# Kernel tuning notes

Hardware: AMD Instinct MI355X
Metric: run time of the kernel (lower is better)

The kernel has to match this reference:

```python
import jax, jax.numpy as jnp
import numpy as np
from jax import lax

D_MODEL = 1024
D_IN = 1024        # expand=1 -> d_inner = d_model
N_STATE = 16       # d_state
DT_RANK = 64       # ceil(d_model/16)
D_FFN = 4096
BATCH, SEQ = 2, 2048


def setup_inputs() -> dict:
    key = jax.random.key(0)
    ks = jax.random.split(key, 12)
    r = lambda i, shape, s=0.02: jax.random.normal(ks[i], shape, jnp.float32) * s
    ones = lambda n: jnp.ones((n,), jnp.float32)
    zeros = lambda n: jnp.zeros((n,), jnp.float32)
    # S4D-real init for A
    A_log = jnp.log(jnp.tile(jnp.arange(1, N_STATE + 1, dtype=jnp.float32), (D_IN, 1)))
    return {
        "src": jax.random.normal(ks[0], (BATCH, SEQ, D_MODEL), jnp.float32),
        "in_proj_w": r(1, (2 * D_IN, D_MODEL)),
        "conv_w": r(2, (D_IN, 2), 0.5),
        "conv_b": zeros(D_IN),
        "x_proj_w": r(3, (DT_RANK + 2 * N_STATE, D_IN)),
        "dt_proj_w": r(4, (D_IN, DT_RANK), 0.1),
        "dt_proj_b": r(5, (D_IN,), 0.1),
        "A_log": A_log,
        "Dp": ones(D_IN),
        "out_proj_w": r(6, (D_MODEL, D_IN)),
        "mnorm_g": ones(D_MODEL), "mnorm_b": zeros(D_MODEL),
        "n1_g": ones(D_MODEL), "n1_b": zeros(D_MODEL),
        "n2_g": ones(D_MODEL), "n2_b": zeros(D_MODEL),
        "n3_g": ones(D_MODEL), "n3_b": zeros(D_MODEL),
        "ffn_w1": r(7, (D_FFN, D_MODEL)),
        "ffn_w2": r(8, (D_MODEL, D_FFN)),
        "fe_w": r(9, (D_MODEL, D_MODEL)),
        "fe_b": zeros(D_MODEL),
    }


def _ln(x, g, b, eps=1e-5):
    m = x.mean(-1, keepdims=True)
    v = ((x - m) ** 2).mean(-1, keepdims=True)
    return (x - m) / jnp.sqrt(v + eps) * g + b


def _mamba(x, in_proj_w, conv_w, conv_b, x_proj_w, dt_proj_w, dt_proj_b,
           A_log, Dp, out_proj_w):
    B, L, _ = x.shape
    xz = x @ in_proj_w.T                       # (B,L,2*D_IN)
    x_in, z = jnp.split(xz, 2, axis=-1)
    # depthwise causal conv1d, kernel size 2: y[l] = w0*x[l-1] + w1*x[l] + b
    x_prev = jnp.pad(x_in, ((0, 0), (1, 0), (0, 0)))[:, :L]
    x_c = jax.nn.silu(x_prev * conv_w[:, 0] + x_in * conv_w[:, 1] + conv_b)
    x_dbl = x_c @ x_proj_w.T                   # (B,L,DT_RANK+2N)
    dt, Bm, Cm = jnp.split(x_dbl, [DT_RANK, DT_RANK + N_STATE], axis=-1)
    delta = jax.nn.softplus(dt @ dt_proj_w.T + dt_proj_b)   # (B,L,D_IN)
    A = -jnp.exp(A_log)                        # (D_IN,N)
    deltaA = jnp.exp(delta[..., None] * A)                   # (B,L,D_IN,N)
    dBu = delta[..., None] * Bm[:, :, None, :] * x_c[..., None]

    def step(h, t):
        dA_t, dBu_t, C_t = t                   # (B,D_IN,N),(B,D_IN,N),(B,N)
        h = dA_t * h + dBu_t
        y = jnp.einsum('bdn,bn->bd', h, C_t)
        return h, y

    h0 = jnp.zeros((B, D_IN, N_STATE), x.dtype)
    _, ys = lax.scan(step, h0,
                     (deltaA.transpose(1, 0, 2, 3),
                      dBu.transpose(1, 0, 2, 3),
                      Cm.transpose(1, 0, 2)))
    y = ys.transpose(1, 0, 2)                  # (B,L,D_IN)
    y = (y + x_c * Dp) * jax.nn.silu(z)
    return y @ out_proj_w.T


def reference(src, in_proj_w, conv_w, conv_b, x_proj_w, dt_proj_w, dt_proj_b,
              A_log, Dp, out_proj_w, mnorm_g, mnorm_b, n1_g, n1_b, n2_g, n2_b,
              n3_g, n3_b, ffn_w1, ffn_w2, fe_w, fe_b):
    # src1 = MambaBlock(norm1(src)); dropout = identity (eval)
    h = _mamba(_ln(src, n1_g, n1_b), in_proj_w, conv_w, conv_b, x_proj_w,
               dt_proj_w, dt_proj_b, A_log, Dp, out_proj_w)
    src = src + _ln(h, mnorm_g, mnorm_b)
    # FFN: Linear -> LeakyReLU(0.01) -> Linear (no bias)
    f = _ln(src, n2_g, n2_b) @ ffn_w1.T
    f = jnp.where(f >= 0, f, 0.01 * f) @ ffn_w2.T
    src = src + f
    src = src + (_ln(src, n3_g, n3_b) @ fe_w.T + fe_b)
    return src
```

## Files before the change

kernel.cpp:

```cpp
#include <hip/hip_runtime.h>
#include <hip/hip_bf16.h>
#include <cstddef>

#define L_SEQ   2048
#define NBATCH  2
#define NROWS   (NBATCH * L_SEQ)
#define NSTATE  16
#define CH      64
#define NCHUNK  (L_SEQ / CH)

typedef __bf16 bf16x8 __attribute__((ext_vector_type(8)));
typedef float  f32x4  __attribute__((ext_vector_type(4)));
typedef unsigned short u16x4 __attribute__((ext_vector_type(4)));

static __device__ __forceinline__ unsigned short f2bf(float f) {
  unsigned int x = __builtin_bit_cast(unsigned int, f);
  x += 0x7fffu + ((x >> 16) & 1u);
  return (unsigned short)(x >> 16);
}
static __device__ __forceinline__ float bf2f(unsigned short u) {
  return __builtin_bit_cast(float, ((unsigned int)u) << 16);
}

#define GLDS(g, l) __builtin_amdgcn_global_load_lds( \
    (const __attribute__((address_space(1))) void*)(g), \
    (__attribute__((address_space(3))) void*)(l), 16, 0, 0)

#define DRAIN_VM() asm volatile("s_waitcnt vmcnt(0)" ::: "memory")

__global__ __launch_bounds__(256) void cvt_bf16_kernel(
    const float* __restrict__ in, unsigned short* __restrict__ out, int n4)
{
  const int i = blockIdx.x * 256 + threadIdx.x;
  if (i < n4) {
    const float4 v = reinterpret_cast<const float4*>(in)[i];
    u16x4 o;
    o[0] = f2bf(v.x); o[1] = f2bf(v.y); o[2] = f2bf(v.z); o[3] = f2bf(v.w);
    reinterpret_cast<u16x4*>(out)[i] = o;
  }
}

__global__ __launch_bounds__(256) void cvt_all_kernel(
    const float* __restrict__ ipw, const float* __restrict__ xpw,
    const float* __restrict__ dtw, const float* __restrict__ opw,
    const float* __restrict__ w1,  const float* __restrict__ w2,
    const float* __restrict__ few,
    unsigned short* __restrict__ o_ipw, unsigned short* __restrict__ o_xpw,
    unsigned short* __restrict__ o_dtw, unsigned short* __restrict__ o_opw,
    unsigned short* __restrict__ o_w1,  unsigned short* __restrict__ o_w2,
    unsigned short* __restrict__ o_few)
{
  int i = blockIdx.x * 256 + threadIdx.x;
  const float* src; unsigned short* dst;
  if (i < 524288)                 { src = ipw; dst = o_ipw; }
  else if ((i -= 524288) < 24576) { src = xpw; dst = o_xpw; }
  else if ((i -= 24576) < 16384)  { src = dtw; dst = o_dtw; }
  else if ((i -= 16384) < 262144) { src = opw; dst = o_opw; }
  else if ((i -= 262144) < 1048576){ src = w1; dst = o_w1; }
  else if ((i -= 1048576) < 1048576){ src = w2; dst = o_w2; }
  else if ((i -= 1048576) < 262144){ src = few; dst = o_few; }
  else return;
  const float4 v = reinterpret_cast<const float4*>(src)[i];
  u16x4 o;
  o[0] = f2bf(v.x); o[1] = f2bf(v.y); o[2] = f2bf(v.z); o[3] = f2bf(v.w);
  reinterpret_cast<u16x4*>(dst)[i] = o;
}

__global__ __launch_bounds__(256) void ln_kernel(
    const float* __restrict__ in, const float* __restrict__ g,
    const float* __restrict__ bta, const float* __restrict__ res,
    float* __restrict__ out, unsigned short* __restrict__ outb)
{
  const int row = blockIdx.x;
  const int tid = threadIdx.x;
  __shared__ float sm[8];
  const float4 v = reinterpret_cast<const float4*>(in + (size_t)row * 1024)[tid];
  float s = v.x + v.y + v.z + v.w;
#pragma unroll
  for (int o = 32; o > 0; o >>= 1) s += __shfl_down(s, o, 64);
  if ((tid & 63) == 0) sm[tid >> 6] = s;
  __syncthreads();
  const float mean = (sm[0] + sm[1] + sm[2] + sm[3]) * (1.f / 1024.f);
  const float dx = v.x - mean, dy = v.y - mean, dz = v.z - mean, dw = v.w - mean;
  float q = dx * dx + dy * dy + dz * dz + dw * dw;
#pragma unroll
  for (int o = 32; o > 0; o >>= 1) q += __shfl_down(q, o, 64);
  __syncthreads();
  if ((tid & 63) == 0) sm[tid >> 6] = q;
  __syncthreads();
  const float var = (sm[0] + sm[1] + sm[2] + sm[3]) * (1.f / 1024.f);
  const float rstd = rsqrtf(var + 1e-5f);
  const float4 gv = reinterpret_cast<const float4*>(g)[tid];
  const float4 bv = reinterpret_cast<const float4*>(bta)[tid];
  float4 o4;
  o4.x = dx * rstd * gv.x + bv.x;
  o4.y = dy * rstd * gv.y + bv.y;
  o4.z = dz * rstd * gv.z + bv.z;
  o4.w = dw * rstd * gv.w + bv.w;
  if (outb) {
    u16x4 ob;
    ob[0] = f2bf(o4.x); ob[1] = f2bf(o4.y); ob[2] = f2bf(o4.z); ob[3] = f2bf(o4.w);
    reinterpret_cast<u16x4*>(outb + (size_t)row * 1024)[tid] = ob;
  } else {
    if (res) {
      const float4 rv = reinterpret_cast<const float4*>(res + (size_t)row * 1024)[tid];
      o4.x += rv.x; o4.y += rv.y; o4.z += rv.z; o4.w += rv.w;
    }
    reinterpret_cast<float4*>(out + (size_t)row * 1024)[tid] = o4;
  }
}

__global__ __launch_bounds__(256) void gemm_bf16_kernel(
    const unsigned short* __restrict__ A, int lda,
    const unsigned short* __restrict__ B, int ldb,
    void* __restrict__ Cv, int ldc,
    const float* __restrict__ bias, const float* __restrict__ res,
    int K, int act, int outbf, int gy)
{
  __shared__ unsigned short As[2][128 * 32];
  __shared__ unsigned short Bs[2][128 * 32];
  const int t = threadIdx.x;
  const int w = t >> 6, l = t & 63;

  const int q = gridDim.x >> 3;
  const int nid = (blockIdx.x & 7) * q + (blockIdx.x >> 3);
  const int bm = (nid / gy) * 128;
  const int bn = (nid % gy) * 128;

  const int wr = (w >> 1) * 64, wc = (w & 1) * 64;
  f32x4 acc[4][4] = {};

  const int srow = t >> 2;
  const int sk = (t & 3) * 8;
  const unsigned short* gA0 = A + (size_t)(bm + srow) * lda + sk;
  const unsigned short* gA1 = gA0 + (size_t)64 * lda;
  const unsigned short* gB0 = B + (size_t)(bn + srow) * ldb + sk;
  const unsigned short* gB1 = gB0 + (size_t)64 * ldb;

  const int fr = l & 15;
  const int kb = (l >> 4) * 8;

#define STAGE(buf, k0) do { \
    GLDS(gA0 + (k0), &As[buf][w * 512]); \
    GLDS(gA1 + (k0), &As[buf][2048 + w * 512]); \
    GLDS(gB0 + (k0), &Bs[buf][w * 512]); \
    GLDS(gB1 + (k0), &Bs[buf][2048 + w * 512]); \
  } while (0)

#define COMPUTE(buf) do { \
    bf16x8 af[4], bfr[4]; \
    _Pragma("unroll") \
    for (int i = 0; i < 4; ++i) \
      af[i] = *reinterpret_cast<const bf16x8*>(&As[buf][(wr + i * 16 + fr) * 32 + kb]); \
    _Pragma("unroll") \
    for (int j = 0; j < 4; ++j) \
      bfr[j] = *reinterpret_cast<const bf16x8*>(&Bs[buf][(wc + j * 16 + fr) * 32 + kb]); \
    _Pragma("unroll") \
    for (int i = 0; i < 4; ++i) \
      _Pragma("unroll") \
      for (int j = 0; j < 4; ++j) \
        acc[i][j] = __builtin_amdgcn_mfma_f32_16x16x32_bf16(af[i], bfr[j], acc[i][j], 0, 0, 0); \
  } while (0)

  STAGE(0, 0);
  DRAIN_VM();
  __syncthreads();
  int cur = 0;
  for (int k0 = 32; k0 < K; k0 += 32) {
    __builtin_amdgcn_sched_barrier(0);
    STAGE(cur ^ 1, k0);
    __builtin_amdgcn_sched_barrier(0);
    COMPUTE(cur);
    DRAIN_VM();
    __syncthreads();
    cur ^= 1;
  }
  COMPUTE(cur);
#undef STAGE
#undef COMPUTE

  const int crow = (l >> 4) * 4;
  const int ccol = l & 15;
  float* Cf = (float*)Cv;
  unsigned short* Cb = (unsigned short*)Cv;
#pragma unroll
  for (int i = 0; i < 4; ++i) {
#pragma unroll
    for (int j = 0; j < 4; ++j) {
      const int n = bn + wc + j * 16 + ccol;
      const float bv = bias ? bias[n] : 0.f;
#pragma unroll
      for (int r = 0; r < 4; ++r) {
        const int m = bm + wr + i * 16 + crow + r;
        float v = acc[i][j][r] + bv;
        if (act == 1) v = (v > 20.f) ? v : __logf(1.f + __expf(v));
        else if (act == 2) v = (v >= 0.f) ? v : 0.01f * v;
        if (res) v += res[(size_t)m * ldc + n];
        if (outbf) Cb[(size_t)m * ldc + n] = f2bf(v);
        else       Cf[(size_t)m * ldc + n] = v;
      }
    }
  }
}

template<int BK>
__global__ __launch_bounds__(512) void gemm_ksplit_kernel(
    const unsigned short* __restrict__ A, int lda,
    const unsigned short* __restrict__ B, int ldb,
    void* __restrict__ Cv, int ldc,
    const float* __restrict__ bias, const float* __restrict__ res,
    int K, int act, int outbf, int gy)
{
  constexpr int ABYTES = 128 * BK * 2;
  constexpr int NISS = (BK == 32) ? 2 : 4;
  constexpr int RPI  = (BK == 32) ? 64 : 32;
  constexpr int NS   = BK / 32;
  __shared__ __align__(16) unsigned char smem[8 * ABYTES];
  const int tid = threadIdx.x;
  const int grp = tid >> 8;
  const int t = tid & 255;
  const int w = t >> 6, l = t & 63;

  const int q = gridDim.x >> 3;
  const int nid = (blockIdx.x & 7) * q + (blockIdx.x >> 3);
  const int bm = (nid / gy) * 128;
  const int bn = (nid % gy) * 128;

  const int K2 = K >> 1;
  const int koff = grp * K2;
  const int wr = (w >> 1) * 64, wc = (w & 1) * 64;
  f32x4 acc[4][4] = {};

  const int srow = (BK == 32) ? (t >> 2) : (t >> 3);
  const int sk   = (BK == 32) ? ((t & 3) * 8) : ((t & 7) * 8);
  const unsigned short* gA = A + (size_t)(bm + srow) * lda + koff + sk;
  const unsigned short* gB = B + (size_t)(bn + srow) * ldb + koff + sk;

  const int gbase = grp * 2 * ABYTES;
  const int fr = l & 15;
  const int kb = (l >> 4) * 8;

#define SAb(buf) (smem + gbase + (buf) * ABYTES)
#define SBb(buf) (smem + 4 * ABYTES + gbase + (buf) * ABYTES)

#define STAGEK(buf, k0) do { \
    _Pragma("unroll") \
    for (int ii = 0; ii < NISS; ++ii) { \
      GLDS(gA + (k0) + (size_t)ii * RPI * lda, SAb(buf) + ii * 4096 + w * 1024); \
      GLDS(gB + (k0) + (size_t)ii * RPI * ldb, SBb(buf) + ii * 4096 + w * 1024); \
    } \
  } while (0)

#define COMPUTEK(buf) do { \
    _Pragma("unroll") \
    for (int s = 0; s < NS; ++s) { \
      bf16x8 af[4], bfr[4]; \
      _Pragma("unroll") \
      for (int i = 0; i < 4; ++i) \
        af[i] = *reinterpret_cast<const bf16x8*>((const unsigned short*)SAb(buf) + (wr + i * 16 + fr) * BK + s * 32 + kb); \
      _Pragma("unroll") \
      for (int j = 0; j < 4; ++j) \
        bfr[j] = *reinterpret_cast<const bf16x8*>((const unsigned short*)SBb(buf) + (wc + j * 16 + fr) * BK + s * 32 + kb); \
      _Pragma("unroll") \
      for (int i = 0; i < 4; ++i) \
        _Pragma("unroll") \
        for (int j = 0; j < 4; ++j) \
          acc[i][j] = __builtin_amdgcn_mfma_f32_16x16x32_bf16(af[i], bfr[j], acc[i][j], 0, 0, 0); \
    } \
  } while (0)

  STAGEK(0, 0);
  DRAIN_VM();
  __syncthreads();
  int cur = 0;
  for (int k0 = BK; k0 < K2; k0 += BK) {
    __builtin_amdgcn_sched_barrier(0);
    STAGEK(cur ^ 1, k0);
    __builtin_amdgcn_sched_barrier(0);
    COMPUTEK(cur);
    DRAIN_VM();
    __syncthreads();
    cur ^= 1;
  }
  COMPUTEK(cur);
#undef STAGEK
#undef COMPUTEK
#undef SAb
#undef SBb

  __syncthreads();
  float* red = (float*)smem;
  if (grp) {
#pragma unroll
    for (int i = 0; i < 4; ++i)
#pragma unroll
      for (int j = 0; j < 4; ++j)
        *reinterpret_cast<f32x4*>(&red[(t << 6) + (i * 4 + j) * 4]) = acc[i][j];
  }
  __syncthreads();
  if (!grp) {
    const int crow = (l >> 4) * 4;
    const int ccol = l & 15;
    float* Cf = (float*)Cv;
    unsigned short* Cb = (unsigned short*)Cv;
#pragma unroll
    for (int i = 0; i < 4; ++i) {
#pragma unroll
      for (int j = 0; j < 4; ++j) {
        const f32x4 o = *reinterpret_cast<const f32x4*>(&red[(t << 6) + (i * 4 + j) * 4]);
        const int n = bn + wc + j * 16 + ccol;
        const float bv = bias ? bias[n] : 0.f;
#pragma unroll
        for (int r = 0; r < 4; ++r) {
          const int m = bm + wr + i * 16 + crow + r;
          float v = acc[i][j][r] + o[r] + bv;
          if (act == 1) v = (v > 20.f) ? v : __logf(1.f + __expf(v));
          else if (act == 2) v = (v >= 0.f) ? v : 0.01f * v;
          if (res) v += res[(size_t)m * ldc + n];
          if (outbf) Cb[(size_t)m * ldc + n] = f2bf(v);
          else       Cf[(size_t)m * ldc + n] = v;
        }
      }
    }
  }
}

__global__ __launch_bounds__(256) void xproj_kernel(
    const unsigned short* __restrict__ A, int lda,
    const unsigned short* __restrict__ B, int ldb,
    float* __restrict__ C)
{
  __shared__ unsigned short As[2][128 * 32];
  __shared__ unsigned short Bs[2][96 * 32];
  const int t = threadIdx.x;
  const int w = t >> 6, l = t & 63;
  const int bm = blockIdx.x * 128;
  const int kbase = blockIdx.y * 128;

  f32x4 acc[2][6] = {};

  const int srow = t >> 2;
  const int sk = (t & 3) * 8;
  const unsigned short* gA0 = A + (size_t)(bm + srow) * lda + kbase + sk;
  const unsigned short* gA1 = gA0 + (size_t)64 * lda;
  const unsigned short* gB0 = B + (size_t)srow * ldb + kbase + sk;
  const unsigned short* gB1 = gB0 + (size_t)64 * ldb;

  const int fr = l & 15;
  const int kb = (l >> 4) * 8;

#define STAGEX(buf, k0) do { \
    GLDS(gA0 + (k0), &As[buf][w * 512]); \
    GLDS(gA1 + (k0), &As[buf][2048 + w * 512]); \
    GLDS(gB0 + (k0), &Bs[buf][w * 512]); \
    if (w < 2) GLDS(gB1 + (k0), &Bs[buf][2048 + w * 512]); \
  } while (0)

#define COMPUTEX(buf) do { \
    bf16x8 af[2], bfr[6]; \
    _Pragma("unroll") \
    for (int i = 0; i < 2; ++i) \
      af[i] = *reinterpret_cast<const bf16x8*>(&As[buf][(w * 32 + i * 16 + fr) * 32 + kb]); \
    _Pragma("unroll") \
    for (int j = 0; j < 6; ++j) \
      bfr[j] = *reinterpret_cast<const bf16x8*>(&Bs[buf][(j * 16 + fr) * 32 + kb]); \
    _Pragma("unroll") \
    for (int i = 0; i < 2; ++i) \
      _Pragma("unroll") \
      for (int j = 0; j < 6; ++j) \
        acc[i][j] = __builtin_amdgcn_mfma_f32_16x16x32_bf16(af[i], bfr[j], acc[i][j], 0, 0, 0); \
  } while (0)

  STAGEX(0, 0);
  DRAIN_VM();
  __syncthreads();
  int cur = 0;
  for (int s = 1; s < 4; ++s) {
    __builtin_amdgcn_sched_barrier(0);
    STAGEX(cur ^ 1, s * 32);
    __builtin_amdgcn_sched_barrier(0);
    COMPUTEX(cur);
    DRAIN_VM();
    __syncthreads();
    cur ^= 1;
  }
  COMPUTEX(cur);
#undef STAGEX
#undef COMPUTEX

  const int crow = (l >> 4) * 4;
  const int ccol = l & 15;
#pragma unroll
  for (int i = 0; i < 2; ++i)
#pragma unroll
    for (int j = 0; j < 6; ++j)
#pragma unroll
      for (int r = 0; r < 4; ++r) {
        const int m = bm + w * 32 + i * 16 + crow + r;
        const int n = j * 16 + ccol;
        atomicAdd(&C[(size_t)m * 96 + n], acc[i][j][r]);
      }
}

__global__ __launch_bounds__(256) void conv_silu_kernel(
    const unsigned short* __restrict__ xz, const float* __restrict__ cw,
    const float* __restrict__ cb, float* __restrict__ xc,
    unsigned short* __restrict__ xcb)
{
  const int idx = blockIdx.x * 256 + threadIdx.x;
  const int row = idx >> 10;
  const int d = idx & 1023;
  const int l = row & (L_SEQ - 1);
  const float cur = bf2f(xz[(size_t)row * 2048 + d]);
  const float prev = (l == 0) ? 0.f : bf2f(xz[(size_t)(row - 1) * 2048 + d]);
  const float v = prev * cw[d * 2 + 0] + cur * cw[d * 2 + 1] + cb[d];
  const float sv = v / (1.f + __expf(-v));
  xc[idx] = sv;
  xcb[idx] = f2bf(sv);
}

__global__ __launch_bounds__(256) void scan_pass1(
    const float* __restrict__ delta, const float* __restrict__ xc,
    const float* __restrict__ xdbl, const float* __restrict__ A_log,
    float* __restrict__ hfin, float* __restrict__ pcum)
{
  const int tid = threadIdx.x;
  const int db = blockIdx.x & 3;
  const int c = (blockIdx.x >> 2) & (NCHUNK - 1);
  const int b = blockIdx.x >> 7;
  const int d = db * 256 + tid;
  __shared__ float Bsh[CH][16];
  {
    const int lr = tid >> 2, q = tid & 3;
    const float* p = xdbl + ((size_t)(b * L_SEQ + c * CH + lr) * 96) + 64 + q * 4;
    *reinterpret_cast<float4*>(&Bsh[lr][q * 4]) = *reinterpret_cast<const float4*>(p);
  }
  float a[NSTATE];
#pragma unroll
  for (int n = 0; n < NSTATE; ++n) a[n] = -__expf(A_log[d * 16 + n]);
  __syncthreads();
  float h[NSTATE], P[NSTATE];
#pragma unroll
  for (int n = 0; n < NSTATE; ++n) { h[n] = 0.f; P[n] = 1.f; }
  const size_t rowbase = (size_t)(b * L_SEQ + c * CH);
  for (int s = 0; s < CH; ++s) {
    const size_t row = rowbase + s;
    const float dl = delta[row * 1024 + d];
    const float xcv = xc[row * 1024 + d];
#pragma unroll
    for (int n = 0; n < NSTATE; ++n) {
      const float dA = __expf(dl * a[n]);
      h[n] = h[n] * dA + (dl * Bsh[s][n]) * xcv;
      P[n] *= dA;
    }
  }
  const size_t base = ((size_t)((b * NCHUNK + c) * 1024 + d)) * 16;
  float4* hp = reinterpret_cast<float4*>(hfin + base);
  float4* pp = reinterpret_cast<float4*>(pcum + base);
#pragma unroll
  for (int qq = 0; qq < 4; ++qq) {
    hp[qq] = make_float4(h[qq * 4], h[qq * 4 + 1], h[qq * 4 + 2], h[qq * 4 + 3]);
    pp[qq] = make_float4(P[qq * 4], P[qq * 4 + 1], P[qq * 4 + 2], P[qq * 4 + 3]);
  }
}

__global__ __launch_bounds__(256) void scan_pass2(
    const float* __restrict__ hfin, const float* __restrict__ pcum,
    float* __restrict__ hstart)
{
  const int t = blockIdx.x * 256 + threadIdx.x;
  const int b = t >> 14;
  const int dn = t & 16383;
  const size_t base = (size_t)b * NCHUNK * 16384 + dn;
  float h = 0.f;
  for (int c = 0; c < NCHUNK; ++c) {
    const size_t idx = base + (size_t)c * 16384;
    hstart[idx] = h;
    h = pcum[idx] * h + hfin[idx];
  }
}

__global__ __launch_bounds__(256) void scan_pass3(
    const float* __restrict__ delta, const float* __restrict__ xc,
    const float* __restrict__ xdbl, const float* __restrict__ A_log,
    const float* __restrict__ hstart, const float* __restrict__ Dp,
    const unsigned short* __restrict__ xz, unsigned short* __restrict__ yout)
{
  const int tid = threadIdx.x;
  const int db = blockIdx.x & 3;
  const int c = (blockIdx.x >> 2) & (NCHUNK - 1);
  const int b = blockIdx.x >> 7;
  const int d = db * 256 + tid;
  __shared__ float Bsh[CH][16];
  __shared__ float Csh[CH][16];
  {
    const int lr = tid >> 2, q = tid & 3;
    const float* p = xdbl + ((size_t)(b * L_SEQ + c * CH + lr) * 96);
    *reinterpret_cast<float4*>(&Bsh[lr][q * 4]) = *reinterpret_cast<const float4*>(p + 64 + q * 4);
    *reinterpret_cast<float4*>(&Csh[lr][q * 4]) = *reinterpret_cast<const float4*>(p + 80 + q * 4);
  }
  float a[NSTATE];
#pragma unroll
  for (int n = 0; n < NSTATE; ++n) a[n] = -__expf(A_log[d * 16 + n]);
  float h[NSTATE];
  {
    const size_t base = ((size_t)((b * NCHUNK + c) * 1024 + d)) * 16;
    const float4* hp = reinterpret_cast<const float4*>(hstart + base);
#pragma unroll
    for (int qq = 0; qq < 4; ++qq) {
      const float4 v = hp[qq];
      h[qq * 4] = v.x; h[qq * 4 + 1] = v.y; h[qq * 4 + 2] = v.z; h[qq * 4 + 3] = v.w;
    }
  }
  const float dpv = Dp[d];
  __syncthreads();
  const size_t rowbase = (size_t)(b * L_SEQ + c * CH);
  for (int s = 0; s < CH; ++s) {
    const size_t row = rowbase + s;
    const float dl = delta[row * 1024 + d];
    const float xcv = xc[row * 1024 + d];
    float y = 0.f;
#pragma unroll
    for (int n = 0; n < NSTATE; ++n) {
      const float dA = __expf(dl * a[n]);
      h[n] = h[n] * dA + (dl * Bsh[s][n]) * xcv;
      y += h[n] * Csh[s][n];
    }
    const float z = bf2f(xz[row * 2048 + 1024 + d]);
    const float sil = z / (1.f + __expf(-z));
    yout[row * 1024 + d] = f2bf((y + xcv * dpv) * sil);
  }
}

extern "C" void kernel_launch(void* const* d_in, const int* in_sizes, int n_in,
                              void* d_out, int out_size, void* d_ws, size_t ws_size,
                              hipStream_t stream)
{
  (void)in_sizes; (void)n_in; (void)out_size; (void)ws_size;
  const float* src        = (const float*)d_in[0];
  const float* in_proj_w  = (const float*)d_in[1];
  const float* conv_w     = (const float*)d_in[2];
  const float* conv_b     = (const float*)d_in[3];
  const float* x_proj_w   = (const float*)d_in[4];
  const float* dt_proj_w  = (const float*)d_in[5];
  const float* dt_proj_b  = (const float*)d_in[6];
  const float* A_log      = (const float*)d_in[7];
  const float* Dp         = (const float*)d_in[8];
  const float* out_proj_w = (const float*)d_in[9];
  const float* mnorm_g    = (const float*)d_in[10];
  const float* mnorm_b    = (const float*)d_in[11];
  const float* n1_g       = (const float*)d_in[12];
  const float* n1_b       = (const float*)d_in[13];
  const float* n2_g       = (const float*)d_in[14];
  const float* n2_b       = (const float*)d_in[15];
  const float* n3_g       = (const float*)d_in[16];
  const float* n3_b       = (const float*)d_in[17];
  const float* ffn_w1     = (const float*)d_in[18];
  const float* ffn_w2     = (const float*)d_in[19];
  const float* fe_w       = (const float*)d_in[20];
  const float* fe_b       = (const float*)d_in[21];
  float* out = (float*)d_out;
  float* ws  = (float*)d_ws;

  unsigned short* xzb  = (unsigned short*)ws;
  unsigned short* xdblb= (unsigned short*)(ws + 4194304);
  unsigned short* dtwb = (unsigned short*)(ws + 4390912);
  float* xc    = ws + 8388608;
  float* xdbl  = ws + 12582912;
  float* delta = ws + 13107200;
  float* s5    = ws + 17301504;
  float* src1  = ws + 21495808;
  float* hfin  = ws + 25690112;
  float* pcum  = ws + 26738688;
  float* hst   = ws + 27787264;
  unsigned short* s1b  = (unsigned short*)(ws + 28835840);
  unsigned short* xcb  = (unsigned short*)(ws + 30932992);
  unsigned short* yb   = (unsigned short*)(ws + 33030144);
  unsigned short* f1b  = (unsigned short*)(ws + 35127296);
  unsigned short* ipwb = (unsigned short*)(ws + 43515904);
  unsigned short* xpwb = (unsigned short*)(ws + 44564480);
  unsigned short* opwb = (unsigned short*)(ws + 44613632);
  unsigned short* w1b  = (unsigned short*)(ws + 45137920);
  unsigned short* w2b  = (unsigned short*)(ws + 47235072);
  unsigned short* fewb = (unsigned short*)(ws + 49332224);

  const dim3 blk(256);
  const dim3 blk512(512);

  cvt_all_kernel<<<12448, blk, 0, stream>>>(
      in_proj_w, x_proj_w, dt_proj_w, out_proj_w, ffn_w1, ffn_w2, fe_w,
      ipwb, xpwb, dtwb, opwb, w1b, w2b, fewb);

  ln_kernel<<<NROWS, blk, 0, stream>>>(src, n1_g, n1_b, nullptr, nullptr, s1b);
  gemm_ksplit_kernel<32><<<512, blk512, 0, stream>>>(s1b, 1024, ipwb, 1024, xzb, 2048,
                                                     nullptr, nullptr, 1024, 0, 1, 16);
  conv_silu_kernel<<<16384, blk, 0, stream>>>(xzb, conv_w, conv_b, xc, xcb);
  hipMemsetAsync(xdbl, 0, (size_t)NROWS * 96 * sizeof(float), stream);
  xproj_kernel<<<dim3(32, 8), blk, 0, stream>>>(xcb, 1024, xpwb, 1024, xdbl);
  cvt_bf16_kernel<<<384, blk, 0, stream>>>(xdbl, xdblb, 98304);
  gemm_bf16_kernel<<<256, blk, 0, stream>>>(xdblb, 96, dtwb, 64, delta, 1024,
                                            dt_proj_b, nullptr, 64, 1, 0, 8);
  scan_pass1<<<256, blk, 0, stream>>>(delta, xc, xdbl, A_log, hfin, pcum);
  scan_pass2<<<128, blk, 0, stream>>>(hfin, pcum, hst);
  scan_pass3<<<256, blk, 0, stream>>>(delta, xc, xdbl, A_log, hst, Dp, xzb, yb);
  gemm_ksplit_kernel<64><<<256, blk512, 0, stream>>>(yb, 1024, opwb, 1024, s5, 1024,
                                                     nullptr, nullptr, 1024, 0, 0, 8);
  ln_kernel<<<NROWS, blk, 0, stream>>>(s5, mnorm_g, mnorm_b, src, src1, nullptr);
  ln_kernel<<<NROWS, blk, 0, stream>>>(src1, n2_g, n2_b, nullptr, nullptr, s1b);
  gemm_bf16_kernel<<<1024, blk, 0, stream>>>(s1b, 1024, w1b, 1024, f1b, 4096,
                                             nullptr, nullptr, 1024, 2, 1, 32);
  gemm_ksplit_kernel<64><<<256, blk512, 0, stream>>>(f1b, 4096, w2b, 4096, s5, 1024,
                                                     nullptr, src1, 4096, 0, 0, 8);
  ln_kernel<<<NROWS, blk, 0, stream>>>(s5, n3_g, n3_b, nullptr, nullptr, s1b);
  gemm_ksplit_kernel<64><<<256, blk512, 0, stream>>>(s1b, 1024, fewb, 1024, out, 1024,
                                                     fe_b, s5, 1024, 0, 0, 8);
}
```

Baseline: 406.5 us.

## Use 256x256 tile GEMM kernel for FFN up-projection

Adds a new 512-thread GEMM kernel with 256x256 output tiles, double-buffered 128KB LDS staging and 8x4 MFMA accumulators per wave, and uses it for the FFN first linear with LeakyReLU and bf16 output. Larger tiles raise arithmetic intensity and cut global/LDS traffic per FLOP compared with the previous 1024-block kernel. The cost is heavy LDS and register use, which limits occupancy to one block per CU, and 256 blocks on a 256-CU device give a single wave of work.

```diff
diff --git a/kernel.cpp b/kernel.cpp
--- a/kernel.cpp
+++ b/kernel.cpp
@@ -185,6 +185,106 @@
   unsigned short* Cb = (unsigned short*)Cv;
 #pragma unroll
   for (int i = 0; i < 4; ++i) {
+#pragma unroll
+    for (int j = 0; j < 4; ++j) {
+      const int n = bn + wc + j * 16 + ccol;
+      const float bv = bias ? bias[n] : 0.f;
+#pragma unroll
+      for (int r = 0; r < 4; ++r) {
+        const int m = bm + wr + i * 16 + crow + r;
+        float v = acc[i][j][r] + bv;
+        if (act == 1) v = (v > 20.f) ? v : __logf(1.f + __expf(v));
+        else if (act == 2) v = (v >= 0.f) ? v : 0.01f * v;
+        if (res) v += res[(size_t)m * ldc + n];
+        if (outbf) Cb[(size_t)m * ldc + n] = f2bf(v);
+        else       Cf[(size_t)m * ldc + n] = v;
+      }
+    }
+  }
+}
+
+__global__ __launch_bounds__(512) void gemm256_kernel(
+    const unsigned short* __restrict__ A, int lda,
+    const unsigned short* __restrict__ B, int ldb,
+    void* __restrict__ Cv, int ldc,
+    const float* __restrict__ bias, const float* __restrict__ res,
+    int K, int act, int outbf, int gy)
+{
+  __shared__ __align__(16) unsigned char smem[131072];
+  const int t = threadIdx.x;
+  const int w = t >> 6, l = t & 63;
+
+  const int q = gridDim.x >> 3;
+  const int nid = (blockIdx.x & 7) * q + (blockIdx.x >> 3);
+  const int bm = (nid / gy) * 256;
+  const int bn = (nid % gy) * 256;
+
+  const int wr = (w >> 2) * 128;
+  const int wc = (w & 3) * 64;
+  f32x4 acc[8][4] = {};
+
+  const int srow = t >> 3;
+  const int sk8 = (t & 7) * 8;
+  const unsigned short* gA = A + (size_t)(bm + srow) * lda + sk8;
+  const unsigned short* gB = B + (size_t)(bn + srow) * ldb + sk8;
+
+  const int fr = l & 15;
+  const int kb = (l >> 4) * 8;
+
+#define SA6(buf) (smem + (buf) * 32768)
+#define SB6(buf) (smem + 65536 + (buf) * 32768)
+
+#define STAGE6(buf, k0) do { \
+    _Pragma("unroll") \
+    for (int ii = 0; ii < 4; ++ii) { \
+      GLDS(gA + (k0) + (size_t)(ii * 64) * lda, SA6(buf) + ii * 8192 + w * 1024); \
+      GLDS(gB + (k0) + (size_t)(ii * 64) * ldb, SB6(buf) + ii * 8192 + w * 1024); \
+    } \
+  } while (0)
+
+#define COMPUTE6(buf) do { \
+    _Pragma("unroll") \
+    for (int s = 0; s < 2; ++s) { \
+      bf16x8 af[8], bfr[4]; \
+      _Pragma("unroll") \
+      for (int j = 0; j < 4; ++j) \
+        bfr[j] = *reinterpret_cast<const bf16x8*>((const unsigned short*)SB6(buf) + (wc + j * 16 + fr) * 64 + s * 32 + kb); \
+      _Pragma("unroll") \
+      for (int i = 0; i < 8; ++i) \
+        af[i] = *reinterpret_cast<const bf16x8*>((const unsigned short*)SA6(buf) + (wr + i * 16 + fr) * 64 + s * 32 + kb); \
+      _Pragma("unroll") \
+      for (int i = 0; i < 8; ++i) \
+        _Pragma("unroll") \
+        for (int j = 0; j < 4; ++j) \
+          acc[i][j] = __builtin_amdgcn_mfma_f32_16x16x32_bf16(af[i], bfr[j], acc[i][j], 0, 0, 0); \
+    } \
+  } while (0)
+
+  STAGE6(0, 0);
+  DRAIN_VM();
+  __syncthreads();
+  int cur = 0;
+  for (int k0 = 64; k0 < K; k0 += 64) {
+    __builtin_amdgcn_sched_barrier(0);
+    STAGE6(cur ^ 1, k0);
+    __builtin_amdgcn_sched_barrier(0);
+    COMPUTE6(cur);
+    DRAIN_VM();
+    __syncthreads();
+    cur ^= 1;
+  }
+  COMPUTE6(cur);
+#undef STAGE6
+#undef COMPUTE6
+#undef SA6
+#undef SB6
+
+  const int crow = (l >> 4) * 4;
+  const int ccol = l & 15;
+  float* Cf = (float*)Cv;
+  unsigned short* Cb = (unsigned short*)Cv;
+#pragma unroll
+  for (int i = 0; i < 8; ++i) {
 #pragma unroll
     for (int j = 0; j < 4; ++j) {
       const int n = bn + wc + j * 16 + ccol;
@@ -607,8 +707,8 @@
                                                      nullptr, nullptr, 1024, 0, 0, 8);
   ln_kernel<<<NROWS, blk, 0, stream>>>(s5, mnorm_g, mnorm_b, src, src1, nullptr);
   ln_kernel<<<NROWS, blk, 0, stream>>>(src1, n2_g, n2_b, nullptr, nullptr, s1b);
-  gemm_bf16_kernel<<<1024, blk, 0, stream>>>(s1b, 1024, w1b, 1024, f1b, 4096,
-                                             nullptr, nullptr, 1024, 2, 1, 32);
+  gemm256_kernel<<<256, blk512, 0, stream>>>(s1b, 1024, w1b, 1024, f1b, 4096,
+                                             nullptr, nullptr, 1024, 2, 1, 16);
   gemm_ksplit_kernel<64><<<256, blk512, 0, stream>>>(f1b, 4096, w2b, 4096, s5, 1024,
                                                      nullptr, src1, 4096, 0, 0, 8);
   ln_kernel<<<NROWS, blk, 0, stream>>>(s5, n3_g, n3_b, nullptr, nullptr, s1b);
```

Measured after the change: 397.5 us. -2.2%, faster.
